# Optimization experiments

Hardware: AMD Instinct MI355X
Metric: run time of the kernel (lower is better)

The kernel has to match this reference:

```python
import jax, jax.numpy as jnp
import numpy as np

PI = 3.141592653589793
EPS = 1e-12  # torch.nn.functional.normalize default eps


def setup_inputs() -> dict:
    key = jax.random.key(0)
    k1, k2, k3, k4 = jax.random.split(key, 4)
    N, D, E, R = 100000, 128, 640000, 500
    z = jax.random.normal(k1, (N, D), dtype=jnp.float32)
    edge_index = jax.random.randint(k2, (2, E), 0, N, dtype=jnp.int64)
    edge_type = jax.random.randint(k3, (E,), 0, R, dtype=jnp.int64)
    # learned relation phases, init uniform(-pi, pi) as in reset_parameters
    phase_rel = jax.random.uniform(k4, (R, D), dtype=jnp.float32, minval=-PI, maxval=PI)
    return {"z": z, "edge_index": edge_index, "edge_type": edge_type, "phase_rel": phase_rel}


def reference(z, edge_index, edge_type, phase_rel):
    # L2-normalize node embeddings along feature dim (torch F.normalize semantics)
    norm = jnp.sqrt(jnp.sum(z * z, axis=1, keepdims=True))
    z = z / jnp.maximum(norm, EPS)
    # z is real (imaginary part zero), rel = exp(i * phase).
    # Re( z_src * rel * conj(z_dst) ) with real z_src, z_dst reduces to
    # z_src * cos(phase) * z_dst  (the sin term multiplies a zero imaginary part).
    z_src = z[edge_index[0]]              # [E, D]
    z_dst = z[edge_index[1]]              # [E, D]
    cos_p = jnp.cos(phase_rel)[edge_type]  # [E, D]
    return jnp.sum(z_src * cos_p * z_dst, axis=1)  # [E]
```

## Files before the change

### kernel.cpp

```cpp
#include <hip/hip_runtime.h>
#include <math.h>

#define D 128
#define EPS_NORM 1e-12f

__device__ __forceinline__ unsigned int f32_to_bf16(float f) {
    unsigned int u = __float_as_uint(f);
    return (u + 0x7FFFu + ((u >> 16) & 1u)) >> 16;
}
__device__ __forceinline__ float bf_lo(unsigned int w) { return __uint_as_float(w << 16); }
__device__ __forceinline__ float bf_hi(unsigned int w) { return __uint_as_float(w & 0xFFFF0000u); }

__global__ void prep_kernel(const float* __restrict__ z, unsigned int* __restrict__ zn, int N,
                            const float* __restrict__ phase, unsigned int* __restrict__ ct, int n2,
                            int nbz) {
    if ((int)blockIdx.x < nbz) {
        int w    = blockIdx.x * 4 + (threadIdx.x >> 6);
        int lane = threadIdx.x & 63;
        int half = lane >> 5;
        int hl   = lane & 31;
        int row  = w * 2 + half;
        if (row >= N) return;
        float4 v = reinterpret_cast<const float4*>(z + (size_t)row * D)[hl];
        float s = v.x * v.x + v.y * v.y + v.z * v.z + v.w * v.w;
#pragma unroll
        for (int off = 16; off > 0; off >>= 1) s += __shfl_xor(s, off, 32);
        float inv = 1.0f / fmaxf(sqrtf(s), EPS_NORM);
        uint2 o;
        o.x = (f32_to_bf16(v.y * inv) << 16) | f32_to_bf16(v.x * inv);
        o.y = (f32_to_bf16(v.w * inv) << 16) | f32_to_bf16(v.z * inv);
        reinterpret_cast<uint2*>(zn + (size_t)row * (D / 2))[hl] = o;
    } else {
        int i = (blockIdx.x - nbz) * blockDim.x + threadIdx.x;
        if (i < n2) {
            float a = cosf(phase[2 * i]);
            float b = cosf(phase[2 * i + 1]);
            ct[i] = (f32_to_bf16(b) << 16) | f32_to_bf16(a);
        }
    }
}

__device__ __forceinline__ float dot8(uint4 sw, uint4 cw, uint4 dw) {
    float p;
    p = bf_lo(sw.x) * bf_lo(cw.x) * bf_lo(dw.x);
    p = fmaf(bf_hi(sw.x) * bf_hi(cw.x), bf_hi(dw.x), p);
    p = fmaf(bf_lo(sw.y) * bf_lo(cw.y), bf_lo(dw.y), p);
    p = fmaf(bf_hi(sw.y) * bf_hi(cw.y), bf_hi(dw.y), p);
    p = fmaf(bf_lo(sw.z) * bf_lo(cw.z), bf_lo(dw.z), p);
    p = fmaf(bf_hi(sw.z) * bf_hi(cw.z), bf_hi(dw.z), p);
    p = fmaf(bf_lo(sw.w) * bf_lo(cw.w), bf_lo(dw.w), p);
    p = fmaf(bf_hi(sw.w) * bf_hi(cw.w), bf_hi(dw.w), p);
    return p;
}

#define ISSUE(S, ev)                                                      \
    int4 S##s = *reinterpret_cast<const int4*>(ei + (ev));                \
    int4 S##d = *reinterpret_cast<const int4*>(ei + E + (ev));            \
    int4 S##t = *reinterpret_cast<const int4*>(et + (ev));                \
    uint4 S##A0 = zn4[(size_t)S##s.x * 16 + l];                           \
    uint4 S##B0 = zn4[(size_t)S##d.x * 16 + l];                           \
    uint4 S##C0 = ct4[(size_t)S##t.x * 16 + l];                           \
    uint4 S##A1 = zn4[(size_t)S##s.y * 16 + l];                           \
    uint4 S##B1 = zn4[(size_t)S##d.y * 16 + l];                           \
    uint4 S##C1 = ct4[(size_t)S##t.y * 16 + l];                           \
    uint4 S##A2 = zn4[(size_t)S##s.z * 16 + l];                           \
    uint4 S##B2 = zn4[(size_t)S##d.z * 16 + l];                           \
    uint4 S##C2 = ct4[(size_t)S##t.z * 16 + l];                           \
    uint4 S##A3 = zn4[(size_t)S##s.w * 16 + l];                           \
    uint4 S##B3 = zn4[(size_t)S##d.w * 16 + l];                           \
    uint4 S##C3 = ct4[(size_t)S##t.w * 16 + l];

#define COMPUTE(S, ebase)                                                 \
    {                                                                     \
        float p0 = dot8(S##A0, S##C0, S##B0);                             \
        float p1 = dot8(S##A1, S##C1, S##B1);                             \
        float p2 = dot8(S##A2, S##C2, S##B2);                             \
        float p3 = dot8(S##A3, S##C3, S##B3);                             \
        _Pragma("unroll")                                                 \
        for (int off = 8; off > 0; off >>= 1) {                           \
            p0 += __shfl_xor(p0, off, 64);                                \
            p1 += __shfl_xor(p1, off, 64);                                \
            p2 += __shfl_xor(p2, off, 64);                                \
            p3 += __shfl_xor(p3, off, 64);                                \
        }                                                                 \
        float v = (l == 0) ? p0 : (l == 1) ? p1 : (l == 2) ? p2 : p3;     \
        if (l < 4) out[(ebase) + l] = v;                                  \
    }

__global__ __launch_bounds__(256, 4) void edge_kernel_v5(
    const unsigned int* __restrict__ zn,
    const unsigned int* __restrict__ ct,
    const int* __restrict__ ei,
    const int* __restrict__ et,
    float* __restrict__ out, int E) {
    const uint4* zn4 = reinterpret_cast<const uint4*>(zn);
    const uint4* ct4 = reinterpret_cast<const uint4*>(ct);
    int tid     = (int)(blockIdx.x * blockDim.x + threadIdx.x);
    int gid     = tid >> 4;
    int l       = threadIdx.x & 15;
    int ngroups = (int)((gridDim.x * blockDim.x) >> 4);
    int stride  = ngroups * 8;
    int E8      = E & ~7;

    for (int e = gid * 8; e + 8 <= E8; e += stride) {
        ISSUE(P, e)
        ISSUE(Q, e + 4)
        asm volatile("" ::: "memory");
        COMPUTE(P, e)
        COMPUTE(Q, e + 4)
    }
    for (int e2 = E8 + gid; e2 < E; e2 += ngroups) {
        int s = ei[e2], dd = ei[E + e2], t = et[e2];
        uint4 A = zn4[(size_t)s * 16 + l];
        uint4 B = zn4[(size_t)dd * 16 + l];
        uint4 C = ct4[(size_t)t * 16 + l];
        float p = dot8(A, C, B);
#pragma unroll
        for (int off = 8; off > 0; off >>= 1) p += __shfl_xor(p, off, 64);
        if (l == 0) out[e2] = p;
    }
}

extern "C" void kernel_launch(void* const* d_in, const int* in_sizes, int n_in,
                              void* d_out, int out_size, void* d_ws, size_t ws_size,
                              hipStream_t stream) {
    const float* z          = (const float*)d_in[0];
    const int*   edge_index = (const int*)d_in[1];
    const int*   edge_type  = (const int*)d_in[2];
    const float* phase_rel  = (const float*)d_in[3];
    float* out = (float*)d_out;

    const int N      = in_sizes[0] / D;
    const int E      = in_sizes[2];
    const int nphase = in_sizes[3];

    const size_t zn_bytes = (size_t)N * (D / 2) * sizeof(unsigned int);

    unsigned int* zn = (unsigned int*)d_ws;
    unsigned int* ct = (unsigned int*)((char*)d_ws + zn_bytes);
    (void)ws_size;

    const int n2  = nphase / 2;
    const int nbz = (N + 7) / 8;
    const int nbc = (n2 + 255) / 256;
    prep_kernel<<<nbz + nbc, 256, 0, stream>>>(z, zn, N, phase_rel, ct, n2, nbz);

    edge_kernel_v5<<<2048, 256, 0, stream>>>(zn, ct, edge_index, edge_type, out, E);
}
```

Baseline: 60.47 us.

## Stage gathered node rows into LDS via direct global-to-LDS loads

Rewrites the edge kernel so each wave handles 8 edges. Their indices are loaded cooperatively and spread with shuffles, and the source and destination bf16 rows are pulled straight into per-wave shared memory with global_load_lds, then read back for the dot products. The launch bound is raised to allow 8 blocks per CU. The aim is to cut vector registers and redundant index loads. In exchange each wave keeps far fewer independent loads in flight than before (8 edges per wave instead of 32), and it adds a full vmcnt wait plus an LDS round trip.

```diff
diff --git a/kernel.cpp b/kernel.cpp
--- a/kernel.cpp
+++ b/kernel.cpp
@@ -3,6 +3,9 @@
 
 #define D 128
 #define EPS_NORM 1e-12f
+
+typedef __attribute__((address_space(3))) unsigned int lds_u32;
+typedef __attribute__((address_space(1))) const unsigned int glb_u32;
 
 __device__ __forceinline__ unsigned int f32_to_bf16(float f) {
     unsigned int u = __float_as_uint(f);
@@ -53,71 +56,80 @@
     return p;
 }
 
-#define ISSUE(S, ev)                                                      \
-    int4 S##s = *reinterpret_cast<const int4*>(ei + (ev));                \
-    int4 S##d = *reinterpret_cast<const int4*>(ei + E + (ev));            \
-    int4 S##t = *reinterpret_cast<const int4*>(et + (ev));                \
-    uint4 S##A0 = zn4[(size_t)S##s.x * 16 + l];                           \
-    uint4 S##B0 = zn4[(size_t)S##d.x * 16 + l];                           \
-    uint4 S##C0 = ct4[(size_t)S##t.x * 16 + l];                           \
-    uint4 S##A1 = zn4[(size_t)S##s.y * 16 + l];                           \
-    uint4 S##B1 = zn4[(size_t)S##d.y * 16 + l];                           \
-    uint4 S##C1 = ct4[(size_t)S##t.y * 16 + l];                           \
-    uint4 S##A2 = zn4[(size_t)S##s.z * 16 + l];                           \
-    uint4 S##B2 = zn4[(size_t)S##d.z * 16 + l];                           \
-    uint4 S##C2 = ct4[(size_t)S##t.z * 16 + l];                           \
-    uint4 S##A3 = zn4[(size_t)S##s.w * 16 + l];                           \
-    uint4 S##B3 = zn4[(size_t)S##d.w * 16 + l];                           \
-    uint4 S##C3 = ct4[(size_t)S##t.w * 16 + l];
-
-#define COMPUTE(S, ebase)                                                 \
-    {                                                                     \
-        float p0 = dot8(S##A0, S##C0, S##B0);                             \
-        float p1 = dot8(S##A1, S##C1, S##B1);                             \
-        float p2 = dot8(S##A2, S##C2, S##B2);                             \
-        float p3 = dot8(S##A3, S##C3, S##B3);                             \
-        _Pragma("unroll")                                                 \
-        for (int off = 8; off > 0; off >>= 1) {                           \
-            p0 += __shfl_xor(p0, off, 64);                                \
-            p1 += __shfl_xor(p1, off, 64);                                \
-            p2 += __shfl_xor(p2, off, 64);                                \
-            p3 += __shfl_xor(p3, off, 64);                                \
-        }                                                                 \
-        float v = (l == 0) ? p0 : (l == 1) ? p1 : (l == 2) ? p2 : p3;     \
-        if (l < 4) out[(ebase) + l] = v;                                  \
-    }
-
-__global__ __launch_bounds__(256, 4) void edge_kernel_v5(
+__global__ __launch_bounds__(256, 8) void edge_kernel_v6(
     const unsigned int* __restrict__ zn,
     const unsigned int* __restrict__ ct,
     const int* __restrict__ ei,
     const int* __restrict__ et,
     float* __restrict__ out, int E) {
+    __shared__ __align__(16) unsigned int smem[4 * 1024];
+    const uint4* ct4 = reinterpret_cast<const uint4*>(ct);
     const uint4* zn4 = reinterpret_cast<const uint4*>(zn);
-    const uint4* ct4 = reinterpret_cast<const uint4*>(ct);
-    int tid     = (int)(blockIdx.x * blockDim.x + threadIdx.x);
-    int gid     = tid >> 4;
-    int l       = threadIdx.x & 15;
-    int ngroups = (int)((gridDim.x * blockDim.x) >> 4);
-    int stride  = ngroups * 8;
-    int E8      = E & ~7;
 
-    for (int e = gid * 8; e + 8 <= E8; e += stride) {
-        ISSUE(P, e)
-        ISSUE(Q, e + 4)
-        asm volatile("" ::: "memory");
-        COMPUTE(P, e)
-        COMPUTE(Q, e + 4)
+    int wave = (int)(threadIdx.x >> 6);
+    int lane = (int)(threadIdx.x & 63);
+    int l16  = lane & 15;
+    int g    = lane >> 4;
+    unsigned int* wb = smem + wave * 1024;
+
+    int gwid   = (int)((blockIdx.x * blockDim.x + threadIdx.x) >> 6);
+    int nwaves = (int)((gridDim.x * blockDim.x) >> 6);
+    int E8     = E & ~7;
+
+    for (int e = gwid * 8; e + 8 <= E8; e += nwaves * 8) {
+        int idx = 0;
+        if (lane < 8)       idx = ei[e + lane];
+        else if (lane < 16) idx = ei[E + e + (lane - 8)];
+        else if (lane < 24) idx = et[e + (lane - 16)];
+
+        int r  = lane >> 4;
+        int sA = __shfl(idx, r);
+        int sB = __shfl(idx, 4 + r);
+        int dA = __shfl(idx, 8 + r);
+        int dB = __shfl(idx, 12 + r);
+
+        const char* znb = (const char*)zn;
+        size_t off = (size_t)(l16 * 16);
+        __builtin_amdgcn_global_load_lds((glb_u32*)(znb + (size_t)sA * 256 + off), (lds_u32*)(wb + 0),   16, 0, 0);
+        __builtin_amdgcn_global_load_lds((glb_u32*)(znb + (size_t)sB * 256 + off), (lds_u32*)(wb + 256), 16, 0, 0);
+        __builtin_amdgcn_global_load_lds((glb_u32*)(znb + (size_t)dA * 256 + off), (lds_u32*)(wb + 512), 16, 0, 0);
+        __builtin_amdgcn_global_load_lds((glb_u32*)(znb + (size_t)dB * 256 + off), (lds_u32*)(wb + 768), 16, 0, 0);
+
+        int t0 = __shfl(idx, 16 + 2 * g);
+        int t1 = __shfl(idx, 16 + 2 * g + 1);
+        uint4 C0 = ct4[(size_t)t0 * 16 + l16];
+        uint4 C1 = ct4[(size_t)t1 * 16 + l16];
+
+        asm volatile("s_waitcnt vmcnt(0)" ::: "memory");
+
+        int j0 = 2 * g, j1 = 2 * g + 1;
+        uint4 A0 = *reinterpret_cast<const uint4*>(wb + j0 * 64 + l16 * 4);
+        uint4 B0 = *reinterpret_cast<const uint4*>(wb + 512 + j0 * 64 + l16 * 4);
+        float p0 = dot8(A0, C0, B0);
+        uint4 A1 = *reinterpret_cast<const uint4*>(wb + j1 * 64 + l16 * 4);
+        uint4 B1 = *reinterpret_cast<const uint4*>(wb + 512 + j1 * 64 + l16 * 4);
+        float p1 = dot8(A1, C1, B1);
+#pragma unroll
+        for (int o = 8; o > 0; o >>= 1) {
+            p0 += __shfl_xor(p0, o, 64);
+            p1 += __shfl_xor(p1, o, 64);
+        }
+        if (l16 == 0) {
+            out[e + j0] = p0;
+            out[e + j1] = p1;
+        }
     }
-    for (int e2 = E8 + gid; e2 < E; e2 += ngroups) {
+    int ngroups = nwaves * 4;
+    int gidx    = gwid * 4 + g;
+    for (int e2 = E8 + gidx; e2 < E; e2 += ngroups) {
         int s = ei[e2], dd = ei[E + e2], t = et[e2];
-        uint4 A = zn4[(size_t)s * 16 + l];
-        uint4 B = zn4[(size_t)dd * 16 + l];
-        uint4 C = ct4[(size_t)t * 16 + l];
+        uint4 A = zn4[(size_t)s * 16 + l16];
+        uint4 B = zn4[(size_t)dd * 16 + l16];
+        uint4 C = ct4[(size_t)t * 16 + l16];
         float p = dot8(A, C, B);
 #pragma unroll
-        for (int off = 8; off > 0; off >>= 1) p += __shfl_xor(p, off, 64);
-        if (l == 0) out[e2] = p;
+        for (int o = 8; o > 0; o >>= 1) p += __shfl_xor(p, o, 64);
+        if (l16 == 0) out[e2] = p;
     }
 }
 
@@ -145,5 +157,5 @@
     const int nbc = (n2 + 255) / 256;
     prep_kernel<<<nbz + nbc, 256, 0, stream>>>(z, zn, N, phase_rel, ct, n2, nbz);
 
-    edge_kernel_v5<<<2048, 256, 0, stream>>>(zn, ct, edge_index, edge_type, out, E);
+    edge_kernel_v6<<<2048, 256, 0, stream>>>(zn, ct, edge_index, edge_type, out, E);
 }
```

Result: no change. 60.78 us (+0.5%).
